# Kernel tuning notes

Measured on AMD Instinct MI355X. Metric: run time of the kernel, lower is better.

Reference implementation:

```python
import jax, jax.numpy as jnp
import numpy as np
import math

HEADS = 8
CODEBOOK = 1024


def _row_order(h):
    # fftshift-center-out row ordering used by custom_flatten (static, numpy)
    c = h // 2
    order = [c]
    for i in range(1, h):
        if c + i < h:
            order.append(c + i)
        if c - i >= 0:
            order.append(c - i)
    return np.array(order, dtype=np.int32)


def _rope(x):
    # additive-RoPE table: returns x*cos + rotate_half(x)*sin; x: [B, nh, N, d]
    N, d = x.shape[-2], x.shape[-1]
    half = d // 2
    pos = jnp.arange(N, dtype=x.dtype)[:, None]
    div = jnp.exp(jnp.arange(half, dtype=x.dtype) * (-math.log(10000.0) / half))
    emb = pos * div                                   # [N, d/2]
    sin = jnp.tile(jnp.sin(emb), (1, 2))              # [N, d]
    cos = jnp.tile(jnp.cos(emb), (1, 2))
    x1, x2 = x[..., :half], x[..., half:]
    rot = jnp.concatenate([-x2, x1], axis=-1)
    return x * cos + rot * sin


def _ln(x, g, b):
    m = x.mean(-1, keepdims=True)
    v = x.var(-1, keepdims=True)
    return (x - m) / jnp.sqrt(v + 1e-5) * g + b


def _attn(x, qw, qb, pw, pb):
    B, N, D = x.shape
    hd = D // HEADS
    qkv = (x @ qw.T + qb).reshape(B, N, 3, HEADS, hd).transpose(2, 0, 3, 1, 4)
    q, k, v = qkv[0], qkv[1], qkv[2]
    # NOTE: source adds the rotated tensor to the original (q = q + rope(q))
    q = q + _rope(q)
    k = k + _rope(k)
    s = jnp.einsum('bhqd,bhkd->bhqk', q, k) * (hd ** -0.5)
    mask = jnp.triu(jnp.ones((N, N), dtype=bool), 1)
    s = jnp.where(mask, -jnp.inf, s)
    a = jax.nn.softmax(s, axis=-1)
    o = jnp.einsum('bhqk,bhkd->bhqd', a, v).transpose(0, 2, 1, 3).reshape(B, N, D)
    return o @ pw.T + pb


def setup_inputs() -> dict:
    key = jax.random.key(0)
    ks = iter(jax.random.split(key, 64))
    def nrm(shape, s=0.02):
        return jax.random.normal(next(ks), shape, jnp.float32) * s
    Hd, C, L = 1024, 16, 8
    inp = {}
    inp['x'] = nrm((2, C, 64, 64), 1.0)          # post-VAE latent
    inp['condition'] = nrm((2,), 1.0)
    inp['init_w'] = nrm((Hd, 2 * C)); inp['init_b'] = jnp.zeros((Hd,), jnp.float32)
    inp['dc_w'] = nrm((Hd, 1)); inp['dc_b'] = jnp.zeros((Hd,), jnp.float32)
    inp['ln1_g'] = jnp.ones((L, Hd), jnp.float32); inp['ln1_b'] = jnp.zeros((L, Hd), jnp.float32)
    inp['qkv_w'] = nrm((L, 3 * Hd, Hd)); inp['qkv_b'] = jnp.zeros((L, 3 * Hd), jnp.float32)
    inp['proj_w'] = nrm((L, Hd, Hd)); inp['proj_b'] = jnp.zeros((L, Hd), jnp.float32)
    inp['ln2_g'] = jnp.ones((L, Hd), jnp.float32); inp['ln2_b'] = jnp.zeros((L, Hd), jnp.float32)
    inp['ff1_w'] = nrm((L, 4 * Hd, Hd)); inp['ff1_b'] = jnp.zeros((L, 4 * Hd), jnp.float32)
    inp['ff2_w'] = nrm((L, Hd, 4 * Hd)); inp['ff2_b'] = jnp.zeros((L, Hd), jnp.float32)
    inp['mag_w'] = nrm((CODEBOOK * C, Hd // 2)); inp['mag_b'] = jnp.zeros((CODEBOOK * C,), jnp.float32)
    inp['phase_w'] = nrm((CODEBOOK * C, Hd // 2)); inp['phase_b'] = jnp.zeros((CODEBOOK * C,), jnp.float32)
    return inp


def reference(x, condition, init_w, init_b, dc_w, dc_b, ln1_g, ln1_b,
              qkv_w, qkv_b, proj_w, proj_b, ln2_g, ln2_b,
              ff1_w, ff1_b, ff2_w, ff2_b, mag_w, mag_b, phase_w, phase_b):
    xf = jnp.fft.fftshift(jnp.fft.rfft2(x, norm='ortho'), axes=2)
    mag, ph = jnp.real(xf), jnp.imag(xf)
    b, c, h, w = mag.shape
    ro = _row_order(h)
    # custom_flatten == gather rows in center-out order, then flatten
    magf = mag[:, :, ro, :].reshape(b, c, h * w)
    phf = ph[:, :, ro, :].reshape(b, c, h * w)
    t = jnp.stack([magf, phf], axis=1).transpose(0, 3, 1, 2).reshape(b, h * w, 2 * c)
    t = t @ init_w.T + init_b                                   # [b, N, Hd]
    first = condition[:, None, None] * dc_w[:, 0] + dc_b        # [b, 1, Hd]
    t = jnp.concatenate([first, t[:, :-1, :]], axis=1)
    for l in range(qkv_w.shape[0]):
        t = t + _attn(_ln(t, ln1_g[l], ln1_b[l]), qkv_w[l], qkv_b[l], proj_w[l], proj_b[l])
        h2 = _ln(t, ln2_g[l], ln2_b[l])
        t = t + (jax.nn.gelu(h2 @ ff1_w[l].T + ff1_b[l], approximate=False) @ ff2_w[l].T + ff2_b[l])
    Hd = t.shape[-1]
    t4 = t.reshape(b, h * w, 2, Hd // 2)
    # source applies proj to both halves then slices [:, :, 0/1, :]; equivalent to projecting the slice
    mag_logits = (t4[:, :, 0, :] @ mag_w.T + mag_b).reshape(b, h * w, CODEBOOK, c).transpose(0, 3, 2, 1)
    phase_logits = (t4[:, :, 1, :] @ phase_w.T + phase_b).reshape(b, h * w, CODEBOOK, c).transpose(0, 3, 2, 1)
    return (mag_logits, phase_logits)
```

## Files before the change

kernel.cpp:

```cpp
#include <hip/hip_runtime.h>
#include <hip/hip_fp16.h>


typedef _Float16 f16;
typedef _Float16 f16x2 __attribute__((ext_vector_type(2)));
typedef _Float16 f16x4 __attribute__((ext_vector_type(4)));
typedef _Float16 f16x8 __attribute__((ext_vector_type(8)));
typedef float f32x4 __attribute__((ext_vector_type(4)));

#define DEV __device__ __forceinline__

DEV void load_lds16(const f16* g, f16* l) {
  __builtin_amdgcn_global_load_lds((const __attribute__((address_space(1))) void*)(g),
                                   (__attribute__((address_space(3))) void*)(l), 16, 0, 0);
}

__global__ __launch_bounds__(256) void fft_feat_kernel(const float* __restrict__ x,
                                                       float* __restrict__ feat) {
  const int img = blockIdx.x;
  const int b = img >> 4, c = img & 15;
  __shared__ float xs[64 * 64];
  __shared__ float wre[64 * 33];
  __shared__ float wim[64 * 33];
  __shared__ float ct[64];
  __shared__ float st[64];
  const int tid = threadIdx.x;
  if (tid < 64) {
    float th = 0.09817477042468103f * (float)tid;
    ct[tid] = cosf(th);
    st[tid] = sinf(th);
  }
  const float* xp = x + (size_t)img * 4096;
  for (int i = tid; i < 4096; i += 256) xs[i] = xp[i];
  __syncthreads();
  for (int i = tid; i < 64 * 33; i += 256) {
    int y = i / 33, kx = i - y * 33;
    float re = 0.f, im = 0.f;
    for (int xx = 0; xx < 64; ++xx) {
      float v = xs[y * 64 + xx];
      int idx = (kx * xx) & 63;
      re += v * ct[idx];
      im -= v * st[idx];
    }
    wre[i] = re;
    wim[i] = im;
  }
  __syncthreads();
  for (int i = tid; i < 64 * 33; i += 256) {
    int r = i / 33, kx = i - r * 33;
    int row;
    if (r == 0)      row = 32;
    else if (r == 63) row = 0;
    else if (r & 1)  row = 32 + (r + 1) / 2;
    else             row = 32 - r / 2;
    int ky = (row + 32) & 63;
    float re = 0.f, im = 0.f;
    for (int y = 0; y < 64; ++y) {
      int idx = (ky * y) & 63;
      float cr = ct[idx], sr = st[idx];
      float ar = wre[y * 33 + kx], ai = wim[y * 33 + kx];
      re += ar * cr + ai * sr;
      im += ai * cr - ar * sr;
    }
    re *= (1.0f / 64.0f);
    im *= (1.0f / 64.0f);
    float* fb = feat + ((size_t)b * 2112 + i) * 32;
    fb[c] = re;
    fb[16 + c] = im;
  }
}

__global__ __launch_bounds__(256) void init_shift_kernel(
    const float* __restrict__ feat, const float* __restrict__ iw,
    const float* __restrict__ ib, const float* __restrict__ cond,
    const float* __restrict__ dcw, const float* __restrict__ dcb,
    float* __restrict__ t) {
  const int idx = blockIdx.x * 256 + threadIdx.x;
  if (idx >= 2 * 2112 * 1024) return;
  const int d = idx & 1023;
  const int bp = idx >> 10;
  const int b = bp / 2112, p = bp - b * 2112;
  float v;
  if (p == 0) {
    v = cond[b] * dcw[d] + dcb[d];
  } else {
    const float4* f4 = (const float4*)(feat + ((size_t)b * 2112 + (p - 1)) * 32);
    const float4* w4 = (const float4*)(iw + (size_t)d * 32);
    float acc = ib[d];
#pragma unroll
    for (int k = 0; k < 8; ++k) {
      const float4 a = f4[k], w = w4[k];
      acc += a.x * w.x + a.y * w.y + a.z * w.z + a.w * w.w;
    }
    v = acc;
  }
  t[idx] = v;
}

__global__ __launch_bounds__(256) void f32_to_f16_kernel(const float* __restrict__ in,
                                                         f16* __restrict__ out,
                                                         const int n4) {
  int i = blockIdx.x * 256 + threadIdx.x;
  const int stride = gridDim.x * 256;
  for (; i < n4; i += stride) {
    const float4 v = ((const float4*)in)[i];
    f16x4 o;
    o[0] = (f16)v.x; o[1] = (f16)v.y; o[2] = (f16)v.z; o[3] = (f16)v.w;
    ((f16x4*)out)[i] = o;
  }
}

__global__ __launch_bounds__(256) void convert4_kernel(
    const float* __restrict__ s0, f16* __restrict__ d0, const int n0,
    const float* __restrict__ s1, f16* __restrict__ d1, const int n1,
    const float* __restrict__ s2, f16* __restrict__ d2, const int n2,
    const float* __restrict__ s3, f16* __restrict__ d3, const int n3) {
  int i = blockIdx.x * 256 + threadIdx.x;
  const int total = n0 + n1 + n2 + n3;
  const int stride = gridDim.x * 256;
  for (; i < total; i += stride) {
    const float* s; f16* d; int j = i;
    if (j < n0)            { s = s0; d = d0; }
    else { j -= n0; if (j < n1) { s = s1; d = d1; }
    else { j -= n1; if (j < n2) { s = s2; d = d2; }
    else { j -= n2;          s = s3; d = d3; } } }
    const float4 v = ((const float4*)s)[j];
    f16x4 o;
    o[0] = (f16)v.x; o[1] = (f16)v.y; o[2] = (f16)v.z; o[3] = (f16)v.w;
    ((f16x4*)d)[j] = o;
  }
}

__global__ __launch_bounds__(256) void ln_kernel(const float* __restrict__ tin,
                                                 const float* __restrict__ g,
                                                 const float* __restrict__ bb,
                                                 f16* __restrict__ outp) {
  const int row = blockIdx.x;
  const int tid = threadIdx.x, lane = tid & 63, wid = tid >> 6;
  const float4 v = ((const float4*)(tin + (size_t)row * 1024))[tid];
  float s = v.x + v.y + v.z + v.w;
  float s2 = v.x * v.x + v.y * v.y + v.z * v.z + v.w * v.w;
#pragma unroll
  for (int o = 32; o; o >>= 1) {
    s += __shfl_down(s, o);
    s2 += __shfl_down(s2, o);
  }
  __shared__ float red[8];
  if (lane == 0) { red[wid] = s; red[4 + wid] = s2; }
  __syncthreads();
  const float mean = (red[0] + red[1] + red[2] + red[3]) * (1.f / 1024.f);
  const float var = (red[4] + red[5] + red[6] + red[7]) * (1.f / 1024.f) - mean * mean;
  const float rstd = rsqrtf(var + 1e-5f);
  const float4 gv = ((const float4*)g)[tid];
  const float4 bv = ((const float4*)bb)[tid];
  f16x4 o;
  o[0] = (f16)((v.x - mean) * rstd * gv.x + bv.x);
  o[1] = (f16)((v.y - mean) * rstd * gv.y + bv.y);
  o[2] = (f16)((v.z - mean) * rstd * gv.z + bv.z);
  o[3] = (f16)((v.w - mean) * rstd * gv.w + bv.w);
  ((f16x4*)(outp + (size_t)row * 1024))[tid] = o;
}

__global__ __launch_bounds__(256) void rope_split_kernel(const f16* __restrict__ qkv,
                                                         f16* __restrict__ qr,
                                                         f16* __restrict__ kr,
                                                         f16* __restrict__ vt) {
  const int z = blockIdx.y;
  const int pt = blockIdx.x;
  const int b = z >> 3, h = z & 7;
  const int p0 = pt * 64;
  const int tid = threadIdx.x;
  __shared__ f16 vtile[64][130];

  for (int it = 0; it < 8; ++it) {
    int idx = it * 256 + tid;
    int pr = idx >> 5, dp = idx & 31;
    int dh = dp * 2;
    int p = p0 + pr;
    const size_t base = ((size_t)(b * 2112 + p)) * 3072 + h * 128;
    float sn0, cs0, sn1, cs1;
    {
      float div0 = expf((float)dh * -0.14391156831212787f);
      float div1 = expf((float)(dh + 1) * -0.14391156831212787f);
      sincosf((float)p * div0, &sn0, &cs0);
      sincosf((float)p * div1, &sn1, &cs1);
    }
    {
      const f16x2 a = *(const f16x2*)(qkv + base + dh);
      const f16x2 c = *(const f16x2*)(qkv + base + 64 + dh);
      f16x2 lo, hi;
      lo[0] = (f16)((float)a[0] + (float)a[0] * cs0 - (float)c[0] * sn0);
      lo[1] = (f16)((float)a[1] + (float)a[1] * cs1 - (float)c[1] * sn1);
      hi[0] = (f16)((float)c[0] + (float)c[0] * cs0 + (float)a[0] * sn0);
      hi[1] = (f16)((float)c[1] + (float)c[1] * cs1 + (float)a[1] * sn1);
      f16* qo = qr + ((size_t)z * 2112 + p) * 128;
      *(f16x2*)(qo + dh) = lo;
      *(f16x2*)(qo + 64 + dh) = hi;
    }
    {
      const f16x2 a = *(const f16x2*)(qkv + base + 1024 + dh);
      const f16x2 c = *(const f16x2*)(qkv + base + 1024 + 64 + dh);
      f16x2 lo, hi;
      lo[0] = (f16)((float)a[0] + (float)a[0] * cs0 - (float)c[0] * sn0);
      lo[1] = (f16)((float)a[1] + (float)a[1] * cs1 - (float)c[1] * sn1);
      hi[0] = (f16)((float)c[0] + (float)c[0] * cs0 + (float)a[0] * sn0);
      hi[1] = (f16)((float)c[1] + (float)c[1] * cs1 + (float)a[1] * sn1);
      f16* ko = kr + ((size_t)z * 2112 + p) * 128;
      *(f16x2*)(ko + dh) = lo;
      *(f16x2*)(ko + 64 + dh) = hi;
    }
    {
      *(f16x2*)(&vtile[pr][dh]) = *(const f16x2*)(qkv + base + 2048 + dh);
      *(f16x2*)(&vtile[pr][64 + dh]) = *(const f16x2*)(qkv + base + 2048 + 64 + dh);
    }
  }
  __syncthreads();
  for (int it = 0; it < 16; ++it) {
    int idx = it * 256 + tid;
    int d = idx >> 5, pcp = idx & 31;
    int pc = pcp * 2;
    f16x2 o;
    o[0] = vtile[pc][d];
    o[1] = vtile[pc + 1][d];
    *(f16x2*)(vt + ((size_t)z * 128 + d) * 2112 + p0 + pc) = o;
  }
}

__global__ __launch_bounds__(256) void softmax_kernel(f16* S) {
  const int z = blockIdx.y, q = blockIdx.x;
  f16* row = S + ((size_t)z * 2112 + q) * 2112;
  const int valid = q + 1;
  const int fill0 = ((q >> 7) + 1) << 7;
  const int fill = fill0 < 2112 ? fill0 : 2112;
  const int nchunk = fill >> 3;
  __shared__ float buf[2112];
  __shared__ float red[4];
  const int tid = threadIdx.x, lane = tid & 63, wid = tid >> 6;
  float m = -1e30f;
  for (int c = tid; c * 8 < valid; c += 256) {
    const f16x8 v8 = *(const f16x8*)(row + c * 8);
#pragma unroll
    for (int e = 0; e < 8; ++e) {
      const int i = c * 8 + e;
      const float v = (float)v8[e];
      if (i < valid) { buf[i] = v; m = fmaxf(m, v); }
    }
  }
#pragma unroll
  for (int o = 32; o; o >>= 1) m = fmaxf(m, __shfl_down(m, o));
  if (lane == 0) red[wid] = m;
  __syncthreads();
  m = fmaxf(fmaxf(red[0], red[1]), fmaxf(red[2], red[3]));
  __syncthreads();
  float s = 0.f;
  for (int i = tid; i < valid; i += 256) {
    const float e = expf(buf[i] - m);
    buf[i] = e;
    s += e;
  }
#pragma unroll
  for (int o = 32; o; o >>= 1) s += __shfl_down(s, o);
  if (lane == 0) red[wid] = s;
  __syncthreads();
  const float inv = 1.f / (red[0] + red[1] + red[2] + red[3]);
  for (int c = tid; c < nchunk; c += 256) {
    f16x8 o;
#pragma unroll
    for (int e = 0; e < 8; ++e) {
      const int i = c * 8 + e;
      o[e] = (i < valid) ? (f16)(buf[i] * inv) : (f16)0.f;
    }
    *(f16x8*)(row + c * 8) = o;
  }
}

template <int MODE>
__global__ __launch_bounds__(256) void gemm_f16(
    const f16* __restrict__ A, const f16* __restrict__ B,
    const int M, const int N, const int K, const int lda, const int ldb,
    const long sA, const long sB,
    const float* __restrict__ bias,
    float* outF, f16* outH, const float* res, const int ldc) {
  const int tn = blockIdx.x, tm = blockIdx.y, z = blockIdx.z;
  const int m0 = tm * 128, n0 = tn * 128;
  if (MODE == 4 && n0 > m0 + 127) return;
  const f16* Ab = A + (size_t)z * sA;
  const f16* Bb = B + (size_t)z * sB;
  __shared__ __align__(16) f16 Ash[4096];
  __shared__ __align__(16) f16 Bsh[4096];
  const int tid = threadIdx.x;
  const int wave = tid >> 6, lane = tid & 63;
  const int wr = wave >> 1, wc = wave & 1;

  f32x4 acc[4][4];
#pragma unroll
  for (int i = 0; i < 4; ++i)
#pragma unroll
    for (int j = 0; j < 4; ++j)
#pragma unroll
      for (int r = 0; r < 4; ++r) acc[i][j][r] = 0.f;

  const int srow = wave * 16 + (lane >> 2);
  const int scol = (lane & 3) * 8;
  const int ldsoff = wave * 512 + lane * 8;
  const int arow = lane & 15, kg = lane >> 4;

  const int Kend = (MODE == 5) ? (K < m0 + 128 ? K : m0 + 128) : K;

  for (int k0 = 0; k0 < Kend; k0 += 32) {
#pragma unroll
    for (int s = 0; s < 2; ++s) {
      int ar = m0 + srow + s * 64; ar = ar < M ? ar : M - 1;
      load_lds16(Ab + (size_t)ar * lda + k0 + scol, Ash + s * 2048 + ldsoff);
      int br = n0 + srow + s * 64; br = br < N ? br : N - 1;
      load_lds16(Bb + (size_t)br * ldb + k0 + scol, Bsh + s * 2048 + ldsoff);
    }
    __syncthreads();
    f16x8 af[4], bf[4];
#pragma unroll
    for (int i = 0; i < 4; ++i)
      af[i] = *(const f16x8*)(Ash + (wr * 64 + i * 16 + arow) * 32 + kg * 8);
#pragma unroll
    for (int j = 0; j < 4; ++j)
      bf[j] = *(const f16x8*)(Bsh + (wc * 64 + j * 16 + arow) * 32 + kg * 8);
#pragma unroll
    for (int i = 0; i < 4; ++i)
#pragma unroll
      for (int j = 0; j < 4; ++j)
        acc[i][j] = __builtin_amdgcn_mfma_f32_16x16x32_f16(af[i], bf[j], acc[i][j], 0, 0, 0);
    __syncthreads();
  }

#pragma unroll
  for (int i = 0; i < 4; ++i) {
#pragma unroll
    for (int r = 0; r < 4; ++r) {
      const int m = m0 + wr * 64 + i * 16 + (lane >> 4) * 4 + r;
#pragma unroll
      for (int j = 0; j < 4; ++j) {
        const int n = n0 + wc * 64 + j * 16 + (lane & 15);
        float v = acc[i][j][r];
        if (MODE == 0) {
          if (m < M && n < N) outF[(size_t)m * ldc + n] = v + bias[n];
        } else if (MODE == 1) {
          if (m < M && n < N) {
            float t0 = res[(size_t)m * ldc + n];
            outF[(size_t)m * ldc + n] = v + bias[n] + t0;
          }
        } else if (MODE == 2) {
          if (m < M && n < N) {
            float g0 = v + bias[n];
            g0 = 0.5f * g0 * (1.f + erff(g0 * 0.70710678118654752f));
            outH[(size_t)m * ldc + n] = (f16)g0;
          }
        } else if (MODE == 3) {
          if (m < M && n < N) {
            int code = m >> 4, ci = m & 15;
            int bb2 = (n >= 2112) ? 1 : 0;
            int p = n - bb2 * 2112;
            outF[((size_t)(bb2 * 16 + ci) * 1024 + code) * 2112 + p] = v + bias[m];
          }
        } else if (MODE == 4) {
          if (m < M && n < N)
            outH[(size_t)z * 4460544 + (size_t)m * 2112 + n] =
                (f16)(v * 0.08838834764831845f);
        } else if (MODE == 5) {
          int bb2 = z >> 3, h = z & 7;
          if (m < M && n < N)
            outH[((size_t)(bb2 * 2112 + m)) * 1024 + h * 128 + n] = (f16)v;
        } else {
          if (m < M && n < N) outH[(size_t)m * ldc + n] = (f16)(v + bias[n]);
        }
      }
    }
  }
}

extern "C" void kernel_launch(void* const* d_in, const int* in_sizes, int n_in,
                              void* d_out, int out_size, void* d_ws, size_t ws_size,
                              hipStream_t stream) {
  const float* x      = (const float*)d_in[0];
  const float* cond   = (const float*)d_in[1];
  const float* init_w = (const float*)d_in[2];
  const float* init_b = (const float*)d_in[3];
  const float* dc_w   = (const float*)d_in[4];
  const float* dc_b   = (const float*)d_in[5];
  const float* ln1_g  = (const float*)d_in[6];
  const float* ln1_b  = (const float*)d_in[7];
  const float* qkv_w  = (const float*)d_in[8];
  const float* qkv_b  = (const float*)d_in[9];
  const float* proj_w = (const float*)d_in[10];
  const float* proj_b = (const float*)d_in[11];
  const float* ln2_g  = (const float*)d_in[12];
  const float* ln2_b  = (const float*)d_in[13];
  const float* ff1_w  = (const float*)d_in[14];
  const float* ff1_b  = (const float*)d_in[15];
  const float* ff2_w  = (const float*)d_in[16];
  const float* ff2_b  = (const float*)d_in[17];
  const float* mag_w  = (const float*)d_in[18];
  const float* mag_b  = (const float*)d_in[19];
  const float* phase_w = (const float*)d_in[20];
  const float* phase_b = (const float*)d_in[21];

  char* ws = (char*)d_ws;
  size_t off = 0;
  auto alloc = [&](size_t bytes) -> void* {
    void* p = ws + off;
    off += (bytes + 255) & ~(size_t)255;
    return p;
  };
  float* feat = (float*)alloc((size_t)2 * 2112 * 32 * 4);
  float* t    = (float*)alloc((size_t)4224 * 1024 * 4);
  f16* tln    = (f16*)alloc((size_t)4224 * 1024 * 2);
  f16* qkvh   = (f16*)alloc((size_t)4224 * 3072 * 2);
  f16* qr     = (f16*)alloc((size_t)16 * 2112 * 128 * 2);
  f16* kr     = (f16*)alloc((size_t)16 * 2112 * 128 * 2);
  f16* vt     = (f16*)alloc((size_t)16 * 2112 * 128 * 2);
  f16* S      = (f16*)alloc((size_t)16 * 2112 * 2112 * 2);
  f16* ao     = (f16*)alloc((size_t)4224 * 1024 * 2);
  f16* ffh    = (f16*)alloc((size_t)4224 * 4096 * 2);
  f16* tf16   = (f16*)alloc((size_t)4224 * 1024 * 2);
  f16* wq     = (f16*)alloc((size_t)3145728 * 2);
  f16* wp     = (f16*)alloc((size_t)1048576 * 2);
  f16* w1     = (f16*)alloc((size_t)4194304 * 2);
  f16* w2     = (f16*)alloc((size_t)4194304 * 2);
  f16* wh     = (f16*)alloc((size_t)8388608 * 2);
  (void)ws_size; (void)n_in; (void)in_sizes; (void)out_size;

  fft_feat_kernel<<<32, 256, 0, stream>>>(x, feat);
  init_shift_kernel<<<16896, 256, 0, stream>>>(feat, init_w, init_b, cond, dc_w, dc_b, t);

  for (int l = 0; l < 8; ++l) {
    convert4_kernel<<<2048, 256, 0, stream>>>(
        qkv_w + (size_t)l * 3145728, wq, 3145728 / 4,
        proj_w + (size_t)l * 1048576, wp, 1048576 / 4,
        ff1_w + (size_t)l * 4194304, w1, 4194304 / 4,
        ff2_w + (size_t)l * 4194304, w2, 4194304 / 4);

    ln_kernel<<<4224, 256, 0, stream>>>(t, ln1_g + l * 1024, ln1_b + l * 1024, tln);
    gemm_f16<6><<<dim3(24, 33, 1), 256, 0, stream>>>(
        tln, wq, 4224, 3072, 1024, 1024, 1024, 0, 0,
        qkv_b + l * 3072, nullptr, qkvh, nullptr, 3072);
    rope_split_kernel<<<dim3(33, 16), 256, 0, stream>>>(qkvh, qr, kr, vt);
    gemm_f16<4><<<dim3(17, 17, 16), 256, 0, stream>>>(
        qr, kr, 2112, 2112, 128, 128, 128, (long)2112 * 128, (long)2112 * 128,
        nullptr, nullptr, S, nullptr, 0);
    softmax_kernel<<<dim3(2112, 16), 256, 0, stream>>>(S);
    gemm_f16<5><<<dim3(1, 17, 16), 256, 0, stream>>>(
        S, vt, 2112, 128, 2112, 2112, 2112, (long)2112 * 2112, (long)128 * 2112,
        nullptr, nullptr, ao, nullptr, 0);
    gemm_f16<1><<<dim3(8, 33, 1), 256, 0, stream>>>(
        ao, wp, 4224, 1024, 1024, 1024, 1024, 0, 0,
        proj_b + l * 1024, t, nullptr, t, 1024);

    ln_kernel<<<4224, 256, 0, stream>>>(t, ln2_g + l * 1024, ln2_b + l * 1024, tln);
    gemm_f16<2><<<dim3(32, 33, 1), 256, 0, stream>>>(
        tln, w1, 4224, 4096, 1024, 1024, 1024, 0, 0,
        ff1_b + l * 4096, nullptr, ffh, nullptr, 4096);
    gemm_f16<1><<<dim3(8, 33, 1), 256, 0, stream>>>(
        ffh, w2, 4224, 1024, 4096, 4096, 4096, 0, 0,
        ff2_b + l * 1024, t, nullptr, t, 1024);
  }

  f32_to_f16_kernel<<<1024, 256, 0, stream>>>(t, tf16, (4224 * 1024) / 4);

  f32_to_f16_kernel<<<2048, 256, 0, stream>>>(mag_w, wh, 8388608 / 4);
  gemm_f16<3><<<dim3(33, 128, 1), 256, 0, stream>>>(
      wh, tf16, 16384, 4224, 512, 512, 1024, 0, 0,
      mag_b, (float*)d_out, nullptr, nullptr, 0);

  f32_to_f16_kernel<<<2048, 256, 0, stream>>>(phase_w, wh, 8388608 / 4);
  gemm_f16<3><<<dim3(33, 128, 1), 256, 0, stream>>>(
      wh, tf16 + 512, 16384, 4224, 512, 512, 1024, 0, 0,
      phase_b, (float*)d_out + 69206016, nullptr, nullptr, 0);
}
```

Before: 5.225 ms.

## Fuse QK^T, softmax and PV into a flash-attention kernel

Replaces the three-step attention (score GEMM writing a full f16 score matrix, a separate softmax pass, then the PV GEMM) with one fused kernel. It uses online softmax over 64-key tiles, swizzled LDS tiles for K and V, and MFMA for both products. The goal is to remove the large score-matrix write and re-read and two kernel launches per layer. The trade-off is a small grid (17x16 blocks) with heavy register use and causal work that varies by block, which is why query tiles are issued in reverse order.

```diff
diff --git a/kernel.cpp b/kernel.cpp
--- a/kernel.cpp
+++ b/kernel.cpp
@@ -226,52 +226,166 @@
   }
 }
 
-__global__ __launch_bounds__(256) void softmax_kernel(f16* S) {
-  const int z = blockIdx.y, q = blockIdx.x;
-  f16* row = S + ((size_t)z * 2112 + q) * 2112;
-  const int valid = q + 1;
-  const int fill0 = ((q >> 7) + 1) << 7;
-  const int fill = fill0 < 2112 ? fill0 : 2112;
-  const int nchunk = fill >> 3;
-  __shared__ float buf[2112];
-  __shared__ float red[4];
-  const int tid = threadIdx.x, lane = tid & 63, wid = tid >> 6;
-  float m = -1e30f;
-  for (int c = tid; c * 8 < valid; c += 256) {
-    const f16x8 v8 = *(const f16x8*)(row + c * 8);
-#pragma unroll
-    for (int e = 0; e < 8; ++e) {
-      const int i = c * 8 + e;
-      const float v = (float)v8[e];
-      if (i < valid) { buf[i] = v; m = fmaxf(m, v); }
-    }
-  }
-#pragma unroll
-  for (int o = 32; o; o >>= 1) m = fmaxf(m, __shfl_down(m, o));
-  if (lane == 0) red[wid] = m;
-  __syncthreads();
-  m = fmaxf(fmaxf(red[0], red[1]), fmaxf(red[2], red[3]));
-  __syncthreads();
-  float s = 0.f;
-  for (int i = tid; i < valid; i += 256) {
-    const float e = expf(buf[i] - m);
-    buf[i] = e;
-    s += e;
-  }
-#pragma unroll
-  for (int o = 32; o; o >>= 1) s += __shfl_down(s, o);
-  if (lane == 0) red[wid] = s;
-  __syncthreads();
-  const float inv = 1.f / (red[0] + red[1] + red[2] + red[3]);
-  for (int c = tid; c < nchunk; c += 256) {
-    f16x8 o;
-#pragma unroll
-    for (int e = 0; e < 8; ++e) {
-      const int i = c * 8 + e;
-      o[e] = (i < valid) ? (f16)(buf[i] * inv) : (f16)0.f;
-    }
-    *(f16x8*)(row + c * 8) = o;
-  }
+__global__ __launch_bounds__(256) void attn_kernel(
+    const f16* __restrict__ qr, const f16* __restrict__ kr,
+    const f16* __restrict__ vt, f16* __restrict__ ao) {
+  const int qt = (int)gridDim.x - 1 - (int)blockIdx.x;
+  const int z = blockIdx.y;
+  const int b = z >> 3, h = z & 7;
+  const int tid = threadIdx.x, wave = tid >> 6, lane = tid & 63;
+  const int arow = lane & 15, lg = lane >> 4;
+  const int mloc = wave * 32;
+
+  __shared__ __align__(16) f16 Kl[64 * 128];
+  __shared__ __align__(16) f16 Vl[128 * 64];
+  __shared__ __align__(16) f16 Pl[128 * 72];
+
+  const f16* krz = kr + (size_t)z * 270336;
+  const f16* vtz = vt + (size_t)z * 270336;
+
+  f16x8 qf[2][4];
+#pragma unroll
+  for (int i = 0; i < 2; ++i) {
+    int qrow = qt * 128 + mloc + i * 16 + arow;
+    qrow = qrow < 2112 ? qrow : 2111;
+    const f16* qp = qr + ((size_t)z * 2112 + qrow) * 128 + lg * 8;
+#pragma unroll
+    for (int ks = 0; ks < 4; ++ks) qf[i][ks] = *(const f16x8*)(qp + ks * 32);
+  }
+
+  float mrow[2][4], lrow[2][4];
+  f32x4 oacc[2][8];
+#pragma unroll
+  for (int i = 0; i < 2; ++i)
+#pragma unroll
+    for (int r = 0; r < 4; ++r) { mrow[i][r] = -1e30f; lrow[i][r] = 0.f; }
+#pragma unroll
+  for (int i = 0; i < 2; ++i)
+#pragma unroll
+    for (int j = 0; j < 8; ++j)
+#pragma unroll
+      for (int r = 0; r < 4; ++r) oacc[i][j][r] = 0.f;
+
+  const int nt0 = 2 * (qt + 1);
+  const int ntiles = nt0 < 33 ? nt0 : 33;
+  for (int kt = 0; kt < ntiles; ++kt) {
+#pragma unroll
+    for (int s = 0; s < 4; ++s) {
+      const int row = wave * 16 + s * 4 + lg;
+      const int krow = kt * 64 + row;
+      const int sb = (arow * 16) ^ ((row & 7) << 4);
+      load_lds16(krz + (size_t)krow * 128 + (sb >> 1),
+                 Kl + (wave * 16 + s * 4) * 128 + lane * 8);
+    }
+    __syncthreads();
+
+#pragma unroll
+    for (int s = 0; s < 4; ++s) {
+      const int row = wave * 32 + s * 8 + (lane >> 3);
+      const int u = lane & 7;
+      const int sb = (u * 16) ^ ((row & 7) << 4);
+      load_lds16(vtz + (size_t)row * 2112 + (size_t)kt * 64 + (sb >> 1),
+                 Vl + (wave * 32 + s * 8) * 64 + lane * 8);
+    }
+
+    f32x4 sa[2][4];
+#pragma unroll
+    for (int i = 0; i < 2; ++i)
+#pragma unroll
+      for (int j = 0; j < 4; ++j)
+#pragma unroll
+        for (int r = 0; r < 4; ++r) sa[i][j][r] = 0.f;
+#pragma unroll
+    for (int ks = 0; ks < 4; ++ks) {
+      f16x8 bf[4];
+#pragma unroll
+      for (int j = 0; j < 4; ++j) {
+        const int rowk = j * 16 + arow;
+        bf[j] = *(const f16x8*)(Kl + rowk * 128 +
+                                (((ks * 32 + lg * 8)) ^ ((rowk & 7) << 3)));
+      }
+#pragma unroll
+      for (int i = 0; i < 2; ++i)
+#pragma unroll
+        for (int j = 0; j < 4; ++j)
+          sa[i][j] = __builtin_amdgcn_mfma_f32_16x16x32_f16(qf[i][ks], bf[j], sa[i][j], 0, 0, 0);
+    }
+
+    const bool dtile = (kt >= 2 * qt);
+#pragma unroll
+    for (int i = 0; i < 2; ++i)
+#pragma unroll
+      for (int j = 0; j < 4; ++j)
+#pragma unroll
+        for (int r = 0; r < 4; ++r) {
+          float v = sa[i][j][r] * 0.08838834764831845f;
+          if (dtile) {
+            const int n = kt * 64 + j * 16 + arow;
+            const int m = qt * 128 + mloc + i * 16 + lg * 4 + r;
+            if (n > m) v = -1e30f;
+          }
+          sa[i][j][r] = v;
+        }
+
+#pragma unroll
+    for (int i = 0; i < 2; ++i) {
+#pragma unroll
+      for (int r = 0; r < 4; ++r) {
+        float tmax = fmaxf(fmaxf(sa[i][0][r], sa[i][1][r]),
+                           fmaxf(sa[i][2][r], sa[i][3][r]));
+#pragma unroll
+        for (int o = 8; o; o >>= 1) tmax = fmaxf(tmax, __shfl_xor(tmax, o));
+        const float mnew = fmaxf(mrow[i][r], tmax);
+        const float psc = __expf(mrow[i][r] - mnew);
+        float ts = 0.f;
+        const int prow = mloc + i * 16 + lg * 4 + r;
+#pragma unroll
+        for (int j = 0; j < 4; ++j) {
+          const float p = __expf(sa[i][j][r] - mnew);
+          ts += p;
+          Pl[prow * 72 + j * 16 + arow] = (f16)p;
+        }
+#pragma unroll
+        for (int o = 8; o; o >>= 1) ts += __shfl_xor(ts, o);
+        lrow[i][r] = lrow[i][r] * psc + ts;
+        mrow[i][r] = mnew;
+#pragma unroll
+        for (int j = 0; j < 8; ++j) oacc[i][j][r] *= psc;
+      }
+    }
+    __syncthreads();
+
+#pragma unroll
+    for (int ks = 0; ks < 2; ++ks) {
+      f16x8 pa[2];
+#pragma unroll
+      for (int i = 0; i < 2; ++i)
+        pa[i] = *(const f16x8*)(Pl + (mloc + i * 16 + arow) * 72 + ks * 32 + lg * 8);
+#pragma unroll
+      for (int j = 0; j < 8; ++j) {
+        const int rowv = j * 16 + arow;
+        const f16x8 vb = *(const f16x8*)(Vl + rowv * 64 +
+                                         (((ks * 32 + lg * 8)) ^ ((rowv & 7) << 3)));
+#pragma unroll
+        for (int i = 0; i < 2; ++i)
+          oacc[i][j] = __builtin_amdgcn_mfma_f32_16x16x32_f16(pa[i], vb, oacc[i][j], 0, 0, 0);
+      }
+    }
+    __syncthreads();
+  }
+
+#pragma unroll
+  for (int i = 0; i < 2; ++i)
+#pragma unroll
+    for (int r = 0; r < 4; ++r) {
+      const int m = qt * 128 + mloc + i * 16 + lg * 4 + r;
+      if (m < 2112) {
+        const float inv = 1.f / lrow[i][r];
+        f16* op = ao + ((size_t)(b * 2112 + m)) * 1024 + h * 128;
+#pragma unroll
+        for (int j = 0; j < 8; ++j) op[j * 16 + arow] = (f16)(oacc[i][j][r] * inv);
+      }
+    }
 }
 
 template <int MODE>
@@ -283,7 +397,6 @@
     float* outF, f16* outH, const float* res, const int ldc) {
   const int tn = blockIdx.x, tm = blockIdx.y, z = blockIdx.z;
   const int m0 = tm * 128, n0 = tn * 128;
-  if (MODE == 4 && n0 > m0 + 127) return;
   const f16* Ab = A + (size_t)z * sA;
   const f16* Bb = B + (size_t)z * sB;
   __shared__ __align__(16) f16 Ash[4096];
@@ -305,9 +418,7 @@
   const int ldsoff = wave * 512 + lane * 8;
   const int arow = lane & 15, kg = lane >> 4;
 
-  const int Kend = (MODE == 5) ? (K < m0 + 128 ? K : m0 + 128) : K;
-
-  for (int k0 = 0; k0 < Kend; k0 += 32) {
+  for (int k0 = 0; k0 < K; k0 += 32) {
 #pragma unroll
     for (int s = 0; s < 2; ++s) {
       int ar = m0 + srow + s * 64; ar = ar < M ? ar : M - 1;
@@ -360,14 +471,6 @@
             int p = n - bb2 * 2112;
             outF[((size_t)(bb2 * 16 + ci) * 1024 + code) * 2112 + p] = v + bias[m];
           }
-        } else if (MODE == 4) {
-          if (m < M && n < N)
-            outH[(size_t)z * 4460544 + (size_t)m * 2112 + n] =
-                (f16)(v * 0.08838834764831845f);
-        } else if (MODE == 5) {
-          int bb2 = z >> 3, h = z & 7;
-          if (m < M && n < N)
-            outH[((size_t)(bb2 * 2112 + m)) * 1024 + h * 128 + n] = (f16)v;
         } else {
           if (m < M && n < N) outH[(size_t)m * ldc + n] = (f16)(v + bias[n]);
         }
@@ -416,7 +519,6 @@
   f16* qr     = (f16*)alloc((size_t)16 * 2112 * 128 * 2);
   f16* kr     = (f16*)alloc((size_t)16 * 2112 * 128 * 2);
   f16* vt     = (f16*)alloc((size_t)16 * 2112 * 128 * 2);
-  f16* S      = (f16*)alloc((size_t)16 * 2112 * 2112 * 2);
   f16* ao     = (f16*)alloc((size_t)4224 * 1024 * 2);
   f16* ffh    = (f16*)alloc((size_t)4224 * 4096 * 2);
   f16* tf16   = (f16*)alloc((size_t)4224 * 1024 * 2);
@@ -442,13 +544,7 @@
         tln, wq, 4224, 3072, 1024, 1024, 1024, 0, 0,
         qkv_b + l * 3072, nullptr, qkvh, nullptr, 3072);
     rope_split_kernel<<<dim3(33, 16), 256, 0, stream>>>(qkvh, qr, kr, vt);
-    gemm_f16<4><<<dim3(17, 17, 16), 256, 0, stream>>>(
-        qr, kr, 2112, 2112, 128, 128, 128, (long)2112 * 128, (long)2112 * 128,
-        nullptr, nullptr, S, nullptr, 0);
-    softmax_kernel<<<dim3(2112, 16), 256, 0, stream>>>(S);
-    gemm_f16<5><<<dim3(1, 17, 16), 256, 0, stream>>>(
-        S, vt, 2112, 128, 2112, 2112, 2112, (long)2112 * 2112, (long)128 * 2112,
-        nullptr, nullptr, ao, nullptr, 0);
+    attn_kernel<<<dim3(17, 16), 256, 0, stream>>>(qr, kr, vt, ao);
     gemm_f16<1><<<dim3(8, 33, 1), 256, 0, stream>>>(
         ao, wp, 4224, 1024, 1024, 1024, 1024, 0, 0,
         proj_b + l * 1024, t, nullptr, t, 1024);
```

New measurement: 4.995 ms. 1.05x faster.
